# Optimization experiments

Measured on AMD Instinct MI355X. Metric: run time of the kernel, lower is better.

Reference implementation:

```python
import jax, jax.numpy as jnp
import numpy as np
from jax import lax

CONV3_NUM = 5
CONV1_NUM = 1
NEG_SLOPE = 0.2


def _leaky(x):
    return jnp.where(x >= 0, x, NEG_SLOPE * x)


def _per_sample_conv(x, k, b, pad):
    # x: [B,3,H,W], k: [B,3,3,kh,kw] (OIHW per sample), b: [B,3]
    def one(xi, ki, bi):
        y = lax.conv_general_dilated(
            xi[None], ki, (1, 1), ((pad, pad), (pad, pad)),
            dimension_numbers=("NCHW", "OIHW", "NCHW"))[0]
        return y + bi[:, None, None]
    return jax.vmap(one)(x, k, b)


def _conv3x3_block(x, feat):
    B = x.shape[0]
    k = feat[:, :81].reshape(B, 3, 3, 3, 3)
    b = feat[:, 81:84]
    return _leaky(x + _per_sample_conv(x, k, b, 1))


def _conv1x1_block(x, feat):
    B = x.shape[0]
    k = feat[:, :9].reshape(B, 3, 3, 1, 1)
    b = feat[:, 9:12]
    return _leaky(x + _per_sample_conv(x, k, b, 0))


def _att_map(f, h, w, xi):
    # f: [B,20]; h,w: [1,1,H,W]; xi: [B,1,H,W]  -> cubic trivariate polynomial
    c = lambda i: f[:, i][:, None, None, None]
    h2 = h * h; h3 = h2 * h
    w2 = w * w; w3 = w2 * w
    x2 = xi * xi; x3 = x2 * xi
    return (c(0) * h3 + c(1) * h2 * w + c(2) * h2 * xi + c(3) * h2
            + c(4) * h * w2 + c(5) * h * w * xi + c(6) * h * w
            + c(7) * h * x2 + c(8) * h * xi + c(9) * h
            + c(10) * w3 + c(11) * w2 * xi + c(12) * w2
            + c(13) * w * x2 + c(14) * w * xi + c(15) * w
            + c(16) * x3 + c(17) * x2 + c(18) * xi + c(19))


def setup_inputs() -> dict:
    key = jax.random.key(0)
    k1, k2, k3 = jax.random.split(key, 3)
    x = jax.random.normal(k1, (8, 3, 1024, 1024), dtype=jnp.float32)
    thumb_x = jax.random.normal(k2, (8, 3, 256, 256), dtype=jnp.float32)
    # meta() is an external CNN predicting per-sample params; we materialize its
    # output directly (scaled small for numerical stability of the conv stack).
    feature = jax.random.normal(k3, (8, 492), dtype=jnp.float32) * 0.05
    return {"x": x, "thumb_x": thumb_x, "feature": feature}


def reference(x, thumb_x, feature):
    B, _, H, W = x.shape
    residual = x
    for i in range(CONV3_NUM):
        x = _conv3x3_block(x, feature[:, i * 84:(i + 1) * 84])
    off = CONV3_NUM * 84
    for i in range(CONV1_NUM):
        x = _conv1x1_block(x, feature[:, off + i * 12:off + (i + 1) * 12])
    off = off + CONV1_NUM * 12
    x = residual + x
    dt = x.dtype
    h_mat = jnp.broadcast_to((jnp.arange(H, dtype=dt) / H)[None, None, :, None], (1, 1, H, W))
    w_mat = jnp.broadcast_to((jnp.arange(W, dtype=dt) / W)[None, None, None, :], (1, 1, H, W))
    atts = [_att_map(feature[:, off + 20 * c:off + 20 * (c + 1)], h_mat, w_mat, x[:, c:c + 1])
            for c in range(3)]
    att = jnp.concatenate(atts, axis=1)
    x = x * (1 + att)
    # location is None => thumbnail branch is skipped, thumb_x returned as-is
    return (x, thumb_x)
```

## Files before the change

kernel.cpp:

```cpp
#include <hip/hip_runtime.h>
#include <hip/hip_fp16.h>

typedef unsigned int uint;
typedef _Float16 h2 __attribute__((ext_vector_type(2)));


#define ROWS   42
#define W_U    40
#define W_REAL 38
#define CHP_U  (ROWS*W_U)
#define BUF_U  (3*CHP_U)

__device__ __forceinline__ h2   U2H(uint u) { return __builtin_bit_cast(h2, u); }
__device__ __forceinline__ uint H2U(h2 h)   { return __builtin_bit_cast(uint, h); }

__global__ void prep_weights(const float* __restrict__ feat, uint* __restrict__ wtab)
{
    const int b = blockIdx.x;
    const int t = threadIdx.x;
    float w = 0.f;
    bool valid = false;
    if (t < 405) {
        int l = t / 81, r = t % 81;
        int ic = r / 27; r %= 27;
        int ky = r / 9;  r %= 9;
        int oc = r / 3;
        int kx = r % 3;
        w = feat[b * 492 + l * 84 + ((oc * 3 + ic) * 3 + ky) * 3 + kx];
        valid = true;
    } else if (t < 420) {
        int i = t - 405;
        w = feat[b * 492 + (i / 3) * 84 + 81 + (i % 3)];
        valid = true;
    }
    if (valid) {
        _Float16 h = (_Float16)w;
        h2 hh = { h, h };
        wtab[b * 448 + t] = H2U(hh);
    }
}

__global__ __launch_bounds__(512, 8) void fused_net(
    const float* __restrict__ xin,
    const float* __restrict__ thumb,
    const float* __restrict__ feat,
    const uint*  __restrict__ wtab,
    float* __restrict__ out)
{
    const int tid = threadIdx.x;

    if (blockIdx.x == 16) {
        const int part = blockIdx.y + 32 * blockIdx.z;
        const float4* s4 = (const float4*)thumb;
        float4* d4 = (float4*)(out + 25165824ull);
        const int n4 = 1572864 / 4;
        for (int i = part * 512 + tid; i < n4; i += 256 * 512)
            d4[i] = s4[i];
        return;
    }

    const int gx0 = blockIdx.x * 64;
    const int gy0 = blockIdx.y * 32;
    const int b   = blockIdx.z;
    const bool edge = (gx0 == 0) | (gx0 == 960) | (gy0 == 0) | (gy0 == 992);
    const float* wf = feat + b * 492;
    const uint*  wt = wtab + b * 448;

    __shared__ __align__(16) uint lds[2 * BUF_U + 8];
    uint* b0 = lds;
    uint* b1 = lds + BUF_U + 4;

    const float* xb = xin + ((size_t)(b * 3) << 20);
    {
        int srow = tid / 38;
        int su   = tid - srow * 38;
        int sch  = 0;
        if (!edge) {
            #pragma unroll
            for (int it = 0; it < 10; ++it) {
                if (it < 9 || tid < 180) {
                    const float2 f = *(const float2*)(xb + ((size_t)sch << 20) +
                                                      ((size_t)(gy0 - 5 + srow) << 10) +
                                                      (gx0 - 6 + 2 * su));
                    b0[sch * CHP_U + srow * W_U + su] =
                        __builtin_bit_cast(uint, __builtin_amdgcn_cvt_pkrtz(f.x, f.y));
                }
                su += 18; srow += 13;
                if (su >= 38)   { su -= 38; srow += 1; }
                if (srow >= 42) { srow -= 42; sch += 1; }
            }
        } else {
            #pragma unroll
            for (int it = 0; it < 10; ++it) {
                if (it < 9 || tid < 180) {
                    const int gy = gy0 - 5 + srow;
                    const int gx = gx0 - 6 + 2 * su;
                    float2 f = {0.f, 0.f};
                    if ((unsigned)gy < 1024u && (unsigned)gx < 1024u)
                        f = *(const float2*)(xb + ((size_t)sch << 20) +
                                             ((size_t)gy << 10) + gx);
                    b0[sch * CHP_U + srow * W_U + su] =
                        __builtin_bit_cast(uint, __builtin_amdgcn_cvt_pkrtz(f.x, f.y));
                }
                su += 18; srow += 13;
                if (su >= 38)   { su -= 38; srow += 1; }
                if (srow >= 42) { srow -= 42; sch += 1; }
            }
        }
    }
    __syncthreads();

    const int er  = tid >> 5;
    const int uc  = tid & 31;
    const int ub0 = (5 + er) * W_U + 3 + uc;
    const int ub1 = ub0 + 16 * W_U;
    uint resu[2][3];
    #pragma unroll
    for (int ch = 0; ch < 3; ++ch) {
        resu[0][ch] = b0[ch * CHP_U + ub0];
        resu[1][ch] = b0[ch * CHP_U + ub1];
    }

    const int cr = tid / 18;
    const int cc = tid - cr * 18;
    const int y0 = 1 + 2 * cr;
    const int x0 = 2 + 4 * cc;
    uint mA[2] = {~0u, ~0u}, mB[2] = {~0u, ~0u};
    if (edge) {
        const int gyA = gy0 - 5 + y0;
        const int gxA = gx0 - 6 + x0;
        const uint mA0 = ((((unsigned)gxA       < 1024u) ? 0x0000ffffu : 0u) |
                          (((unsigned)(gxA + 1) < 1024u) ? 0xffff0000u : 0u));
        const uint mB0 = ((((unsigned)(gxA + 2) < 1024u) ? 0x0000ffffu : 0u) |
                          (((unsigned)(gxA + 3) < 1024u) ? 0xffff0000u : 0u));
        #pragma unroll
        for (int j = 0; j < 2; ++j) {
            const uint mr = ((unsigned)(gyA + j) < 1024u) ? ~0u : 0u;
            mA[j] = mA0 & mr;
            mB[j] = mB0 & mr;
        }
    }

    const h2 c02 = { (_Float16)0.2f, (_Float16)0.2f };

    #pragma unroll
    for (int l = 0; l < 5; ++l) {
        const uint* sb = (l & 1) ? b1 : b0;
        uint*       db = (l & 1) ? b0 : b1;
        if (tid < 360) {
            const uint* tb = sb + (y0 - 1) * W_U + 2 * cc;
            uint*       ob = db + y0 * W_U + 1 + 2 * cc;
            h2 accA[2][3], accB[2][3];
            #pragma unroll
            for (int oc = 0; oc < 3; ++oc) {
                const h2 bi = U2H(wt[405 + l * 3 + oc]);
                accA[0][oc] = bi; accA[1][oc] = bi;
                accB[0][oc] = bi; accB[1][oc] = bi;
            }
            #pragma unroll
            for (int ic = 0; ic < 3; ++ic) {
                #pragma unroll
                for (int t = 0; t < 4; ++t) {
                    const uint2 P = *(const uint2*)(tb + ic * CHP_U + t * W_U);
                    const uint2 Q = *(const uint2*)(tb + ic * CHP_U + t * W_U + 2);
                    const uint u0 = P.x, u1 = P.y, u2 = Q.x, u3 = Q.y;
                    const h2 X01 = U2H((u0 >> 16) | (u1 << 16));
                    const h2 C1  = U2H(u1);
                    const h2 X12 = U2H((u1 >> 16) | (u2 << 16));
                    const h2 C2  = U2H(u2);
                    const h2 X23 = U2H((u2 >> 16) | (u3 << 16));
                    #pragma unroll
                    for (int j = 0; j < 2; ++j) {
                        const int ky = t - j;
                        if (0 <= ky && ky <= 2) {
                            const int wb = l * 81 + (ic * 3 + ky) * 9;
                            #pragma unroll
                            for (int oc = 0; oc < 3; ++oc) {
                                const h2 w0 = U2H(wt[wb + oc * 3 + 0]);
                                const h2 w1 = U2H(wt[wb + oc * 3 + 1]);
                                const h2 w2 = U2H(wt[wb + oc * 3 + 2]);
                                accA[j][oc] = __builtin_elementwise_fma(w0, X01, accA[j][oc]);
                                accA[j][oc] = __builtin_elementwise_fma(w1, C1,  accA[j][oc]);
                                accA[j][oc] = __builtin_elementwise_fma(w2, X12, accA[j][oc]);
                                accB[j][oc] = __builtin_elementwise_fma(w0, X12, accB[j][oc]);
                                accB[j][oc] = __builtin_elementwise_fma(w1, C2,  accB[j][oc]);
                                accB[j][oc] = __builtin_elementwise_fma(w2, X23, accB[j][oc]);
                            }
                        }
                    }
                    if (t == 1) { accA[0][ic] = accA[0][ic] + C1; accB[0][ic] = accB[0][ic] + C2; }
                    if (t == 2) { accA[1][ic] = accA[1][ic] + C1; accB[1][ic] = accB[1][ic] + C2; }
                }
            }
            if (!edge) {
                #pragma unroll
                for (int j = 0; j < 2; ++j) {
                    #pragma unroll
                    for (int oc = 0; oc < 3; ++oc) {
                        h2 vA = accA[j][oc]; vA = __builtin_elementwise_max(vA, c02 * vA);
                        h2 vB = accB[j][oc]; vB = __builtin_elementwise_max(vB, c02 * vB);
                        ob[oc * CHP_U + j * W_U]     = H2U(vA);
                        ob[oc * CHP_U + j * W_U + 1] = H2U(vB);
                    }
                }
            } else {
                #pragma unroll
                for (int j = 0; j < 2; ++j) {
                    #pragma unroll
                    for (int oc = 0; oc < 3; ++oc) {
                        h2 vA = accA[j][oc]; vA = __builtin_elementwise_max(vA, c02 * vA);
                        h2 vB = accB[j][oc]; vB = __builtin_elementwise_max(vB, c02 * vB);
                        ob[oc * CHP_U + j * W_U]     = H2U(vA) & mA[j];
                        ob[oc * CHP_U + j * W_U + 1] = H2U(vB) & mB[j];
                    }
                }
            }
        }
        __syncthreads();
    }

    float* outb = out + ((size_t)(b * 3) << 20);
    #pragma unroll
    for (int rr = 0; rr < 2; ++rr) {
        const int ub = rr ? ub1 : ub0;
        const int gy = gy0 + er + 16 * rr;
        float x5f[3][2], resf[3][2];
        #pragma unroll
        for (int ch = 0; ch < 3; ++ch) {
            h2 hr = U2H(resu[rr][ch]);
            resf[ch][0] = (float)hr.x; resf[ch][1] = (float)hr.y;
            h2 hx = U2H(b1[ch * CHP_U + ub]);
            x5f[ch][0] = (float)hx.x; x5f[ch][1] = (float)hx.y;
        }
        const float h1 = (float)gy * (1.0f / 1024.0f);
        const float h2v = h1 * h1, h3 = h2v * h1;
        float tmp[3][2];
        #pragma unroll
        for (int j = 0; j < 2; ++j) {
            const float wc = (float)(gx0 + 2 * uc + j) * (1.0f / 1024.0f);
            const float w2 = wc * wc, w3 = w2 * wc;
            const float hw = h1 * wc, h2w = h2v * wc, hw2 = h1 * w2;
            #pragma unroll
            for (int oc = 0; oc < 3; ++oc) {
                float s = x5f[oc][j] + wf[429 + oc]
                        + wf[420 + oc * 3 + 0] * x5f[0][j]
                        + wf[420 + oc * 3 + 1] * x5f[1][j]
                        + wf[420 + oc * 3 + 2] * x5f[2][j];
                s = s >= 0.f ? s : 0.2f * s;
                const float xf = resf[oc][j] + s;
                const float x1 = xf, x2 = x1 * x1, x3 = x2 * x1;
                const float* cf = wf + 432 + oc * 20;
                float att =
                    cf[0] * h3 + cf[1] * h2w + cf[2] * h2v * x1 + cf[3] * h2v +
                    cf[4] * hw2 + cf[5] * hw * x1 + cf[6] * hw + cf[7] * h1 * x2 +
                    cf[8] * h1 * x1 + cf[9] * h1 + cf[10] * w3 + cf[11] * w2 * x1 +
                    cf[12] * w2 + cf[13] * wc * x2 + cf[14] * wc * x1 + cf[15] * wc +
                    cf[16] * x3 + cf[17] * x2 + cf[18] * x1 + cf[19];
                tmp[oc][j] = xf * (1.f + att);
            }
        }
        #pragma unroll
        for (int oc = 0; oc < 3; ++oc) {
            float2 v = {tmp[oc][0], tmp[oc][1]};
            *(float2*)&outb[((size_t)oc << 20) + ((size_t)gy << 10) + (gx0 + 2 * uc)] = v;
        }
    }
}

extern "C" void kernel_launch(void* const* d_in, const int* in_sizes, int n_in,
                              void* d_out, int out_size, void* d_ws, size_t ws_size,
                              hipStream_t stream) {
    const float* x     = (const float*)d_in[0];
    const float* thumb = (const float*)d_in[1];
    const float* feat  = (const float*)d_in[2];
    float* out = (float*)d_out;
    uint* wtab = (uint*)d_ws;

    prep_weights<<<dim3(8), 448, 0, stream>>>(feat, wtab);
    dim3 grid(17, 32, 8);
    fused_net<<<grid, 512, 0, stream>>>(x, thumb, feat, wtab, out);
}
```

Before: 288.4 us.

## Widen tiles to 128 columns and fuse final conv layer with epilogue

Doubles the tile width from 64 to 128 columns using 1024-thread blocks. The halo recomputation overhead per output pixel drops from roughly 42x76 to 42x140 loaded per 32x128 output. The fifth conv layer now applies the 1x1 block, residual and attention polynomial directly from registers and writes global memory. This removes the last LDS write, a barrier and the separate epilogue pass. The cost is larger LDS per block and fewer resident blocks, plus uneven work among threads in the final layer.

```diff
diff --git a/kernel.cpp b/kernel.cpp
--- a/kernel.cpp
+++ b/kernel.cpp
@@ -6,10 +6,11 @@
 
 
 #define ROWS   42
-#define W_U    40
-#define W_REAL 38
+#define W_U    72
+#define W_REAL 70
 #define CHP_U  (ROWS*W_U)
 #define BUF_U  (3*CHP_U)
+#define NST    680
 
 __device__ __forceinline__ h2   U2H(uint u) { return __builtin_bit_cast(h2, u); }
 __device__ __forceinline__ uint H2U(h2 h)   { return __builtin_bit_cast(uint, h); }
@@ -40,7 +41,7 @@
     }
 }
 
-__global__ __launch_bounds__(512, 8) void fused_net(
+__global__ __launch_bounds__(1024, 8) void fused_net(
     const float* __restrict__ xin,
     const float* __restrict__ thumb,
     const float* __restrict__ feat,
@@ -49,20 +50,20 @@
 {
     const int tid = threadIdx.x;
 
-    if (blockIdx.x == 16) {
+    if (blockIdx.x == 8) {
         const int part = blockIdx.y + 32 * blockIdx.z;
         const float4* s4 = (const float4*)thumb;
         float4* d4 = (float4*)(out + 25165824ull);
         const int n4 = 1572864 / 4;
-        for (int i = part * 512 + tid; i < n4; i += 256 * 512)
+        for (int i = part * 1024 + tid; i < n4; i += 256 * 1024)
             d4[i] = s4[i];
         return;
     }
 
-    const int gx0 = blockIdx.x * 64;
+    const int gx0 = blockIdx.x * 128;
     const int gy0 = blockIdx.y * 32;
     const int b   = blockIdx.z;
-    const bool edge = (gx0 == 0) | (gx0 == 960) | (gy0 == 0) | (gy0 == 992);
+    const bool edge = (gx0 == 0) | (gx0 == 896) | (gy0 == 0) | (gy0 == 992);
     const float* wf = feat + b * 492;
     const uint*  wt = wtab + b * 448;
 
@@ -72,27 +73,27 @@
 
     const float* xb = xin + ((size_t)(b * 3) << 20);
     {
-        int srow = tid / 38;
-        int su   = tid - srow * 38;
+        int srow = tid / 70;
+        int su   = tid - srow * 70;
         int sch  = 0;
         if (!edge) {
             #pragma unroll
-            for (int it = 0; it < 10; ++it) {
-                if (it < 9 || tid < 180) {
+            for (int it = 0; it < 9; ++it) {
+                if (it < 8 || tid < 628) {
                     const float2 f = *(const float2*)(xb + ((size_t)sch << 20) +
                                                       ((size_t)(gy0 - 5 + srow) << 10) +
                                                       (gx0 - 6 + 2 * su));
                     b0[sch * CHP_U + srow * W_U + su] =
                         __builtin_bit_cast(uint, __builtin_amdgcn_cvt_pkrtz(f.x, f.y));
                 }
-                su += 18; srow += 13;
-                if (su >= 38)   { su -= 38; srow += 1; }
+                su += 44; srow += 14;
+                if (su >= 70)   { su -= 70; srow += 1; }
                 if (srow >= 42) { srow -= 42; sch += 1; }
             }
         } else {
             #pragma unroll
-            for (int it = 0; it < 10; ++it) {
-                if (it < 9 || tid < 180) {
+            for (int it = 0; it < 9; ++it) {
+                if (it < 8 || tid < 628) {
                     const int gy = gy0 - 5 + srow;
                     const int gx = gx0 - 6 + 2 * su;
                     float2 f = {0.f, 0.f};
@@ -102,29 +103,31 @@
                     b0[sch * CHP_U + srow * W_U + su] =
                         __builtin_bit_cast(uint, __builtin_amdgcn_cvt_pkrtz(f.x, f.y));
                 }
-                su += 18; srow += 13;
-                if (su >= 38)   { su -= 38; srow += 1; }
+                su += 44; srow += 14;
+                if (su >= 70)   { su -= 70; srow += 1; }
                 if (srow >= 42) { srow -= 42; sch += 1; }
             }
         }
     }
     __syncthreads();
 
-    const int er  = tid >> 5;
-    const int uc  = tid & 31;
-    const int ub0 = (5 + er) * W_U + 3 + uc;
-    const int ub1 = ub0 + 16 * W_U;
-    uint resu[2][3];
-    #pragma unroll
-    for (int ch = 0; ch < 3; ++ch) {
-        resu[0][ch] = b0[ch * CHP_U + ub0];
-        resu[1][ch] = b0[ch * CHP_U + ub1];
-    }
-
-    const int cr = tid / 18;
-    const int cc = tid - cr * 18;
+    const int cr = tid / 34;
+    const int cc = tid - cr * 34;
     const int y0 = 1 + 2 * cr;
     const int x0 = 2 + 4 * cc;
+    const bool ep = (tid < NST) & (cr >= 2) & (cr <= 17) & (cc >= 1) & (cc <= 32);
+
+    uint resA[3][2], resB[3][2];
+    if (ep) {
+        #pragma unroll
+        for (int ch = 0; ch < 3; ++ch)
+            #pragma unroll
+            for (int j = 0; j < 2; ++j) {
+                resA[ch][j] = b0[ch * CHP_U + (y0 + j) * W_U + 1 + 2 * cc];
+                resB[ch][j] = b0[ch * CHP_U + (y0 + j) * W_U + 2 + 2 * cc];
+            }
+    }
+
     uint mA[2] = {~0u, ~0u}, mB[2] = {~0u, ~0u};
     if (edge) {
         const int gyA = gy0 - 5 + y0;
@@ -147,9 +150,9 @@
     for (int l = 0; l < 5; ++l) {
         const uint* sb = (l & 1) ? b1 : b0;
         uint*       db = (l & 1) ? b0 : b1;
-        if (tid < 360) {
+        const bool act = (l < 4) ? (tid < NST) : ep;
+        if (act) {
             const uint* tb = sb + (y0 - 1) * W_U + 2 * cc;
-            uint*       ob = db + y0 * W_U + 1 + 2 * cc;
             h2 accA[2][3], accB[2][3];
             #pragma unroll
             for (int oc = 0; oc < 3; ++oc) {
@@ -192,78 +195,87 @@
                     if (t == 2) { accA[1][ic] = accA[1][ic] + C1; accB[1][ic] = accB[1][ic] + C2; }
                 }
             }
-            if (!edge) {
+            #pragma unroll
+            for (int j = 0; j < 2; ++j)
+                #pragma unroll
+                for (int oc = 0; oc < 3; ++oc) {
+                    accA[j][oc] = __builtin_elementwise_max(accA[j][oc], c02 * accA[j][oc]);
+                    accB[j][oc] = __builtin_elementwise_max(accB[j][oc], c02 * accB[j][oc]);
+                }
+
+            if (l < 4) {
+                uint* ob = db + y0 * W_U + 1 + 2 * cc;
+                if (!edge) {
+                    #pragma unroll
+                    for (int j = 0; j < 2; ++j)
+                        #pragma unroll
+                        for (int oc = 0; oc < 3; ++oc) {
+                            ob[oc * CHP_U + j * W_U]     = H2U(accA[j][oc]);
+                            ob[oc * CHP_U + j * W_U + 1] = H2U(accB[j][oc]);
+                        }
+                } else {
+                    #pragma unroll
+                    for (int j = 0; j < 2; ++j)
+                        #pragma unroll
+                        for (int oc = 0; oc < 3; ++oc) {
+                            ob[oc * CHP_U + j * W_U]     = H2U(accA[j][oc]) & mA[j];
+                            ob[oc * CHP_U + j * W_U + 1] = H2U(accB[j][oc]) & mB[j];
+                        }
+                }
+            } else {
+                const int gxA = gx0 - 6 + x0;
+                float* outb = out + ((size_t)(b * 3) << 20);
                 #pragma unroll
                 for (int j = 0; j < 2; ++j) {
-                    #pragma unroll
-                    for (int oc = 0; oc < 3; ++oc) {
-                        h2 vA = accA[j][oc]; vA = __builtin_elementwise_max(vA, c02 * vA);
-                        h2 vB = accB[j][oc]; vB = __builtin_elementwise_max(vB, c02 * vB);
-                        ob[oc * CHP_U + j * W_U]     = H2U(vA);
-                        ob[oc * CHP_U + j * W_U + 1] = H2U(vB);
+                    const int gy = gy0 - 5 + y0 + j;
+                    const float h1 = (float)gy * (1.0f / 1024.0f);
+                    const float h2v = h1 * h1, h3 = h2v * h1;
+                    #pragma unroll
+                    for (int hh = 0; hh < 2; ++hh) {
+                        float x5[3][2], rs[3][2];
+                        #pragma unroll
+                        for (int ch = 0; ch < 3; ++ch) {
+                            const h2 a = hh ? accB[j][ch] : accA[j][ch];
+                            x5[ch][0] = (float)a.x; x5[ch][1] = (float)a.y;
+                            const h2 r = U2H(hh ? resB[ch][j] : resA[ch][j]);
+                            rs[ch][0] = (float)r.x; rs[ch][1] = (float)r.y;
+                        }
+                        float o[3][2];
+                        #pragma unroll
+                        for (int p = 0; p < 2; ++p) {
+                            const float wc = (float)(gxA + 2 * hh + p) * (1.0f / 1024.0f);
+                            const float w2 = wc * wc, w3 = w2 * wc;
+                            const float hw = h1 * wc, h2w = h2v * wc, hw2 = h1 * w2;
+                            #pragma unroll
+                            for (int oc = 0; oc < 3; ++oc) {
+                                float s = x5[oc][p] + wf[429 + oc]
+                                        + wf[420 + oc * 3 + 0] * x5[0][p]
+                                        + wf[420 + oc * 3 + 1] * x5[1][p]
+                                        + wf[420 + oc * 3 + 2] * x5[2][p];
+                                s = s >= 0.f ? s : 0.2f * s;
+                                const float xf = rs[oc][p] + s;
+                                const float x1 = xf, x2 = x1 * x1, x3 = x2 * x1;
+                                const float* cf = wf + 432 + oc * 20;
+                                float att =
+                                    cf[0] * h3 + cf[1] * h2w + cf[2] * h2v * x1 + cf[3] * h2v +
+                                    cf[4] * hw2 + cf[5] * hw * x1 + cf[6] * hw + cf[7] * h1 * x2 +
+                                    cf[8] * h1 * x1 + cf[9] * h1 + cf[10] * w3 + cf[11] * w2 * x1 +
+                                    cf[12] * w2 + cf[13] * wc * x2 + cf[14] * wc * x1 + cf[15] * wc +
+                                    cf[16] * x3 + cf[17] * x2 + cf[18] * x1 + cf[19];
+                                o[oc][p] = xf * (1.f + att);
+                            }
+                        }
+                        #pragma unroll
+                        for (int oc = 0; oc < 3; ++oc) {
+                            float2 v = {o[oc][0], o[oc][1]};
+                            *(float2*)&outb[((size_t)oc << 20) + ((size_t)gy << 10) +
+                                            (gxA + 2 * hh)] = v;
+                        }
                     }
                 }
-            } else {
-                #pragma unroll
-                for (int j = 0; j < 2; ++j) {
-                    #pragma unroll
-                    for (int oc = 0; oc < 3; ++oc) {
-                        h2 vA = accA[j][oc]; vA = __builtin_elementwise_max(vA, c02 * vA);
-                        h2 vB = accB[j][oc]; vB = __builtin_elementwise_max(vB, c02 * vB);
-                        ob[oc * CHP_U + j * W_U]     = H2U(vA) & mA[j];
-                        ob[oc * CHP_U + j * W_U + 1] = H2U(vB) & mB[j];
-                    }
-                }
             }
         }
-        __syncthreads();
-    }
-
-    float* outb = out + ((size_t)(b * 3) << 20);
-    #pragma unroll
-    for (int rr = 0; rr < 2; ++rr) {
-        const int ub = rr ? ub1 : ub0;
-        const int gy = gy0 + er + 16 * rr;
-        float x5f[3][2], resf[3][2];
-        #pragma unroll
-        for (int ch = 0; ch < 3; ++ch) {
-            h2 hr = U2H(resu[rr][ch]);
-            resf[ch][0] = (float)hr.x; resf[ch][1] = (float)hr.y;
-            h2 hx = U2H(b1[ch * CHP_U + ub]);
-            x5f[ch][0] = (float)hx.x; x5f[ch][1] = (float)hx.y;
-        }
-        const float h1 = (float)gy * (1.0f / 1024.0f);
-        const float h2v = h1 * h1, h3 = h2v * h1;
-        float tmp[3][2];
-        #pragma unroll
-        for (int j = 0; j < 2; ++j) {
-            const float wc = (float)(gx0 + 2 * uc + j) * (1.0f / 1024.0f);
-            const float w2 = wc * wc, w3 = w2 * wc;
-            const float hw = h1 * wc, h2w = h2v * wc, hw2 = h1 * w2;
-            #pragma unroll
-            for (int oc = 0; oc < 3; ++oc) {
-                float s = x5f[oc][j] + wf[429 + oc]
-                        + wf[420 + oc * 3 + 0] * x5f[0][j]
-                        + wf[420 + oc * 3 + 1] * x5f[1][j]
-                        + wf[420 + oc * 3 + 2] * x5f[2][j];
-                s = s >= 0.f ? s : 0.2f * s;
-                const float xf = resf[oc][j] + s;
-                const float x1 = xf, x2 = x1 * x1, x3 = x2 * x1;
-                const float* cf = wf + 432 + oc * 20;
-                float att =
-                    cf[0] * h3 + cf[1] * h2w + cf[2] * h2v * x1 + cf[3] * h2v +
-                    cf[4] * hw2 + cf[5] * hw * x1 + cf[6] * hw + cf[7] * h1 * x2 +
-                    cf[8] * h1 * x1 + cf[9] * h1 + cf[10] * w3 + cf[11] * w2 * x1 +
-                    cf[12] * w2 + cf[13] * wc * x2 + cf[14] * wc * x1 + cf[15] * wc +
-                    cf[16] * x3 + cf[17] * x2 + cf[18] * x1 + cf[19];
-                tmp[oc][j] = xf * (1.f + att);
-            }
-        }
-        #pragma unroll
-        for (int oc = 0; oc < 3; ++oc) {
-            float2 v = {tmp[oc][0], tmp[oc][1]};
-            *(float2*)&outb[((size_t)oc << 20) + ((size_t)gy << 10) + (gx0 + 2 * uc)] = v;
-        }
+        if (l < 4) __syncthreads();
     }
 }
 
@@ -277,6 +289,6 @@
     uint* wtab = (uint*)d_ws;
 
     prep_weights<<<dim3(8), 448, 0, stream>>>(feat, wtab);
-    dim3 grid(17, 32, 8);
-    fused_net<<<grid, 512, 0, stream>>>(x, thumb, feat, wtab, out);
+    dim3 grid(9, 32, 8);
+    fused_net<<<grid, 1024, 0, stream>>>(x, thumb, feat, wtab, out);
 }
```

Result: slower. 307.9 us (+6.8%).

## Process two vertical tiles per block with register-prefetched second halo

Applied to the files above, without the earlier changes.

Each block now covers a 64-row strip as two 32-row halves, halving the grid in y. The second half's input halo is loaded from global memory into registers before the first half's conv stack runs, then converted and written to shared memory afterwards, so the load latency overlaps with compute. This costs extra registers (20 floats per thread) and halves the number of blocks, which may reduce occupancy or load balance. The thumbnail copy blocks are rescaled to match the new grid.

```diff
diff --git a/kernel.cpp b/kernel.cpp
--- a/kernel.cpp
+++ b/kernel.cpp
@@ -13,6 +13,10 @@
 
 __device__ __forceinline__ h2   U2H(uint u) { return __builtin_bit_cast(h2, u); }
 __device__ __forceinline__ uint H2U(h2 h)   { return __builtin_bit_cast(uint, h); }
+
+#define ADV_WALK() do { su += 18; srow += 13;                  \
+                        if (su >= 38)   { su -= 38; srow += 1; } \
+                        if (srow >= 42) { srow -= 42; sch += 1; } } while (0)
 
 __global__ void prep_weights(const float* __restrict__ feat, uint* __restrict__ wtab)
 {
@@ -50,19 +54,21 @@
     const int tid = threadIdx.x;
 
     if (blockIdx.x == 16) {
-        const int part = blockIdx.y + 32 * blockIdx.z;
+        const int part = blockIdx.y + 16 * blockIdx.z;
         const float4* s4 = (const float4*)thumb;
         float4* d4 = (float4*)(out + 25165824ull);
         const int n4 = 1572864 / 4;
-        for (int i = part * 512 + tid; i < n4; i += 256 * 512)
+        for (int i = part * 512 + tid; i < n4; i += 128 * 512)
             d4[i] = s4[i];
         return;
     }
 
     const int gx0 = blockIdx.x * 64;
-    const int gy0 = blockIdx.y * 32;
+    const int gy0 = blockIdx.y * 64;
     const int b   = blockIdx.z;
-    const bool edge = (gx0 == 0) | (gx0 == 960) | (gy0 == 0) | (gy0 == 992);
+    const bool xedge = (gx0 == 0) | (gx0 == 960);
+    const bool edge0 = xedge | (blockIdx.y == 0);
+    const bool edge1 = xedge | (blockIdx.y == 15);
     const float* wf = feat + b * 492;
     const uint*  wt = wtab + b * 448;
 
@@ -71,11 +77,12 @@
     uint* b1 = lds + BUF_U + 4;
 
     const float* xb = xin + ((size_t)(b * 3) << 20);
+
     {
         int srow = tid / 38;
         int su   = tid - srow * 38;
         int sch  = 0;
-        if (!edge) {
+        if (!edge0) {
             #pragma unroll
             for (int it = 0; it < 10; ++it) {
                 if (it < 9 || tid < 180) {
@@ -85,9 +92,7 @@
                     b0[sch * CHP_U + srow * W_U + su] =
                         __builtin_bit_cast(uint, __builtin_amdgcn_cvt_pkrtz(f.x, f.y));
                 }
-                su += 18; srow += 13;
-                if (su >= 38)   { su -= 38; srow += 1; }
-                if (srow >= 42) { srow -= 42; sch += 1; }
+                ADV_WALK();
             }
         } else {
             #pragma unroll
@@ -102,167 +107,216 @@
                     b0[sch * CHP_U + srow * W_U + su] =
                         __builtin_bit_cast(uint, __builtin_amdgcn_cvt_pkrtz(f.x, f.y));
                 }
-                su += 18; srow += 13;
-                if (su >= 38)   { su -= 38; srow += 1; }
-                if (srow >= 42) { srow -= 42; sch += 1; }
+                ADV_WALK();
             }
         }
     }
     __syncthreads();
+
+    float2 pre[10];
+    {
+        int srow = tid / 38;
+        int su   = tid - srow * 38;
+        int sch  = 0;
+        const int gyb = gy0 + 27;
+        if (!edge1) {
+            #pragma unroll
+            for (int it = 0; it < 10; ++it) {
+                if (it < 9 || tid < 180)
+                    pre[it] = *(const float2*)(xb + ((size_t)sch << 20) +
+                                               ((size_t)(gyb + srow) << 10) +
+                                               (gx0 - 6 + 2 * su));
+                ADV_WALK();
+            }
+        } else {
+            #pragma unroll
+            for (int it = 0; it < 10; ++it) {
+                pre[it].x = 0.f; pre[it].y = 0.f;
+                if (it < 9 || tid < 180) {
+                    const int gy = gyb + srow;
+                    const int gx = gx0 - 6 + 2 * su;
+                    if ((unsigned)gy < 1024u && (unsigned)gx < 1024u)
+                        pre[it] = *(const float2*)(xb + ((size_t)sch << 20) +
+                                                   ((size_t)gy << 10) + gx);
+                }
+                ADV_WALK();
+            }
+        }
+    }
 
     const int er  = tid >> 5;
     const int uc  = tid & 31;
     const int ub0 = (5 + er) * W_U + 3 + uc;
     const int ub1 = ub0 + 16 * W_U;
-    uint resu[2][3];
-    #pragma unroll
-    for (int ch = 0; ch < 3; ++ch) {
-        resu[0][ch] = b0[ch * CHP_U + ub0];
-        resu[1][ch] = b0[ch * CHP_U + ub1];
-    }
-
     const int cr = tid / 18;
     const int cc = tid - cr * 18;
     const int y0 = 1 + 2 * cr;
     const int x0 = 2 + 4 * cc;
-    uint mA[2] = {~0u, ~0u}, mB[2] = {~0u, ~0u};
-    if (edge) {
-        const int gyA = gy0 - 5 + y0;
-        const int gxA = gx0 - 6 + x0;
-        const uint mA0 = ((((unsigned)gxA       < 1024u) ? 0x0000ffffu : 0u) |
-                          (((unsigned)(gxA + 1) < 1024u) ? 0xffff0000u : 0u));
-        const uint mB0 = ((((unsigned)(gxA + 2) < 1024u) ? 0x0000ffffu : 0u) |
-                          (((unsigned)(gxA + 3) < 1024u) ? 0xffff0000u : 0u));
+
+    const h2 c02 = { (_Float16)0.2f, (_Float16)0.2f };
+    float* outb = out + ((size_t)(b * 3) << 20);
+
+    #pragma unroll 1
+    for (int half = 0; half < 2; ++half) {
+        const int  gy0h  = gy0 + 32 * half;
+        const bool edgeh = half ? edge1 : edge0;
+
+        uint resu[2][3];
         #pragma unroll
-        for (int j = 0; j < 2; ++j) {
-            const uint mr = ((unsigned)(gyA + j) < 1024u) ? ~0u : 0u;
-            mA[j] = mA0 & mr;
-            mB[j] = mB0 & mr;
-        }
-    }
-
-    const h2 c02 = { (_Float16)0.2f, (_Float16)0.2f };
-
-    #pragma unroll
-    for (int l = 0; l < 5; ++l) {
-        const uint* sb = (l & 1) ? b1 : b0;
-        uint*       db = (l & 1) ? b0 : b1;
-        if (tid < 360) {
-            const uint* tb = sb + (y0 - 1) * W_U + 2 * cc;
-            uint*       ob = db + y0 * W_U + 1 + 2 * cc;
-            h2 accA[2][3], accB[2][3];
-            #pragma unroll
-            for (int oc = 0; oc < 3; ++oc) {
-                const h2 bi = U2H(wt[405 + l * 3 + oc]);
-                accA[0][oc] = bi; accA[1][oc] = bi;
-                accB[0][oc] = bi; accB[1][oc] = bi;
-            }
-            #pragma unroll
-            for (int ic = 0; ic < 3; ++ic) {
+        for (int ch = 0; ch < 3; ++ch) {
+            resu[0][ch] = b0[ch * CHP_U + ub0];
+            resu[1][ch] = b0[ch * CHP_U + ub1];
+        }
+
+        uint mA[2] = {~0u, ~0u}, mB[2] = {~0u, ~0u};
+        if (edgeh) {
+            const int gyA = gy0h - 5 + y0;
+            const int gxA = gx0 - 6 + x0;
+            const uint mA0 = ((((unsigned)gxA       < 1024u) ? 0x0000ffffu : 0u) |
+                              (((unsigned)(gxA + 1) < 1024u) ? 0xffff0000u : 0u));
+            const uint mB0 = ((((unsigned)(gxA + 2) < 1024u) ? 0x0000ffffu : 0u) |
+                              (((unsigned)(gxA + 3) < 1024u) ? 0xffff0000u : 0u));
+            #pragma unroll
+            for (int j = 0; j < 2; ++j) {
+                const uint mr = ((unsigned)(gyA + j) < 1024u) ? ~0u : 0u;
+                mA[j] = mA0 & mr;
+                mB[j] = mB0 & mr;
+            }
+        }
+
+        #pragma unroll
+        for (int l = 0; l < 5; ++l) {
+            const uint* sb = (l & 1) ? b1 : b0;
+            uint*       db = (l & 1) ? b0 : b1;
+            if (tid < 360) {
+                const uint* tb = sb + (y0 - 1) * W_U + 2 * cc;
+                uint*       ob = db + y0 * W_U + 1 + 2 * cc;
+                h2 accA[2][3], accB[2][3];
                 #pragma unroll
-                for (int t = 0; t < 4; ++t) {
-                    const uint2 P = *(const uint2*)(tb + ic * CHP_U + t * W_U);
-                    const uint2 Q = *(const uint2*)(tb + ic * CHP_U + t * W_U + 2);
-                    const uint u0 = P.x, u1 = P.y, u2 = Q.x, u3 = Q.y;
-                    const h2 X01 = U2H((u0 >> 16) | (u1 << 16));
-                    const h2 C1  = U2H(u1);
-                    const h2 X12 = U2H((u1 >> 16) | (u2 << 16));
-                    const h2 C2  = U2H(u2);
-                    const h2 X23 = U2H((u2 >> 16) | (u3 << 16));
+                for (int oc = 0; oc < 3; ++oc) {
+                    const h2 bi = U2H(wt[405 + l * 3 + oc]);
+                    accA[0][oc] = bi; accA[1][oc] = bi;
+                    accB[0][oc] = bi; accB[1][oc] = bi;
+                }
+                #pragma unroll
+                for (int ic = 0; ic < 3; ++ic) {
                     #pragma unroll
-                    for (int j = 0; j < 2; ++j) {
-                        const int ky = t - j;
-                        if (0 <= ky && ky <= 2) {
-                            const int wb = l * 81 + (ic * 3 + ky) * 9;
-                            #pragma unroll
-                            for (int oc = 0; oc < 3; ++oc) {
-                                const h2 w0 = U2H(wt[wb + oc * 3 + 0]);
-                                const h2 w1 = U2H(wt[wb + oc * 3 + 1]);
-                                const h2 w2 = U2H(wt[wb + oc * 3 + 2]);
-                                accA[j][oc] = __builtin_elementwise_fma(w0, X01, accA[j][oc]);
-                                accA[j][oc] = __builtin_elementwise_fma(w1, C1,  accA[j][oc]);
-                                accA[j][oc] = __builtin_elementwise_fma(w2, X12, accA[j][oc]);
-                                accB[j][oc] = __builtin_elementwise_fma(w0, X12, accB[j][oc]);
-                                accB[j][oc] = __builtin_elementwise_fma(w1, C2,  accB[j][oc]);
-                                accB[j][oc] = __builtin_elementwise_fma(w2, X23, accB[j][oc]);
+                    for (int t = 0; t < 4; ++t) {
+                        const uint2 P = *(const uint2*)(tb + ic * CHP_U + t * W_U);
+                        const uint2 Q = *(const uint2*)(tb + ic * CHP_U + t * W_U + 2);
+                        const uint u0 = P.x, u1 = P.y, u2 = Q.x, u3 = Q.y;
+                        const h2 X01 = U2H((u0 >> 16) | (u1 << 16));
+                        const h2 C1  = U2H(u1);
+                        const h2 X12 = U2H((u1 >> 16) | (u2 << 16));
+                        const h2 C2  = U2H(u2);
+                        const h2 X23 = U2H((u2 >> 16) | (u3 << 16));
+                        #pragma unroll
+                        for (int j = 0; j < 2; ++j) {
+                            const int ky = t - j;
+                            if (0 <= ky && ky <= 2) {
+                                const int wb = l * 81 + (ic * 3 + ky) * 9;
+                                #pragma unroll
+                                for (int oc = 0; oc < 3; ++oc) {
+                                    const h2 w0 = U2H(wt[wb + oc * 3 + 0]);
+                                    const h2 w1 = U2H(wt[wb + oc * 3 + 1]);
+                                    const h2 w2 = U2H(wt[wb + oc * 3 + 2]);
+                                    accA[j][oc] = __builtin_elementwise_fma(w0, X01, accA[j][oc]);
+                                    accA[j][oc] = __builtin_elementwise_fma(w1, C1,  accA[j][oc]);
+                                    accA[j][oc] = __builtin_elementwise_fma(w2, X12, accA[j][oc]);
+                                    accB[j][oc] = __builtin_elementwise_fma(w0, X12, accB[j][oc]);
+                                    accB[j][oc] = __builtin_elementwise_fma(w1, C2,  accB[j][oc]);
+                                    accB[j][oc] = __builtin_elementwise_fma(w2, X23, accB[j][oc]);
+                                }
                             }
                         }
+                        if (t == 1) { accA[0][ic] = accA[0][ic] + C1; accB[0][ic] = accB[0][ic] + C2; }
+                        if (t == 2) { accA[1][ic] = accA[1][ic] + C1; accB[1][ic] = accB[1][ic] + C2; }
                     }
-                    if (t == 1) { accA[0][ic] = accA[0][ic] + C1; accB[0][ic] = accB[0][ic] + C2; }
-                    if (t == 2) { accA[1][ic] = accA[1][ic] + C1; accB[1][ic] = accB[1][ic] + C2; }
-                }
-            }
-            if (!edge) {
+                }
+                if (!edgeh) {
+                    #pragma unroll
+                    for (int j = 0; j < 2; ++j)
+                        #pragma unroll
+                        for (int oc = 0; oc < 3; ++oc) {
+                            h2 vA = accA[j][oc]; vA = __builtin_elementwise_max(vA, c02 * vA);
+                            h2 vB = accB[j][oc]; vB = __builtin_elementwise_max(vB, c02 * vB);
+                            ob[oc * CHP_U + j * W_U]     = H2U(vA);
+                            ob[oc * CHP_U + j * W_U + 1] = H2U(vB);
+                        }
+                } else {
+                    #pragma unroll
+                    for (int j = 0; j < 2; ++j)
+                        #pragma unroll
+                        for (int oc = 0; oc < 3; ++oc) {
+                            h2 vA = accA[j][oc]; vA = __builtin_elementwise_max(vA, c02 * vA);
+                            h2 vB = accB[j][oc]; vB = __builtin_elementwise_max(vB, c02 * vB);
+                            ob[oc * CHP_U + j * W_U]     = H2U(vA) & mA[j];
+                            ob[oc * CHP_U + j * W_U + 1] = H2U(vB) & mB[j];
+                        }
+                }
+            }
+            __syncthreads();
+        }
+
+        #pragma unroll
+        for (int rr = 0; rr < 2; ++rr) {
+            const int ub = rr ? ub1 : ub0;
+            const int gy = gy0h + er + 16 * rr;
+            float x5f[3][2], resf[3][2];
+            #pragma unroll
+            for (int ch = 0; ch < 3; ++ch) {
+                h2 hr = U2H(resu[rr][ch]);
+                resf[ch][0] = (float)hr.x; resf[ch][1] = (float)hr.y;
+                h2 hx = U2H(b1[ch * CHP_U + ub]);
+                x5f[ch][0] = (float)hx.x; x5f[ch][1] = (float)hx.y;
+            }
+            const float h1 = (float)gy * (1.0f / 1024.0f);
+            const float h2v = h1 * h1, h3 = h2v * h1;
+            float tmp[3][2];
+            #pragma unroll
+            for (int j = 0; j < 2; ++j) {
+                const float wc = (float)(gx0 + 2 * uc + j) * (1.0f / 1024.0f);
+                const float w2 = wc * wc, w3 = w2 * wc;
+                const float hw = h1 * wc, h2w = h2v * wc, hw2 = h1 * w2;
                 #pragma unroll
-                for (int j = 0; j < 2; ++j) {
-                    #pragma unroll
-                    for (int oc = 0; oc < 3; ++oc) {
-                        h2 vA = accA[j][oc]; vA = __builtin_elementwise_max(vA, c02 * vA);
-                        h2 vB = accB[j][oc]; vB = __builtin_elementwise_max(vB, c02 * vB);
-                        ob[oc * CHP_U + j * W_U]     = H2U(vA);
-                        ob[oc * CHP_U + j * W_U + 1] = H2U(vB);
-                    }
-                }
-            } else {
-                #pragma unroll
-                for (int j = 0; j < 2; ++j) {
-                    #pragma unroll
-                    for (int oc = 0; oc < 3; ++oc) {
-                        h2 vA = accA[j][oc]; vA = __builtin_elementwise_max(vA, c02 * vA);
-                        h2 vB = accB[j][oc]; vB = __builtin_elementwise_max(vB, c02 * vB);
-                        ob[oc * CHP_U + j * W_U]     = H2U(vA) & mA[j];
-                        ob[oc * CHP_U + j * W_U + 1] = H2U(vB) & mB[j];
-                    }
-                }
-            }
-        }
-        __syncthreads();
-    }
-
-    float* outb = out + ((size_t)(b * 3) << 20);
-    #pragma unroll
-    for (int rr = 0; rr < 2; ++rr) {
-        const int ub = rr ? ub1 : ub0;
-        const int gy = gy0 + er + 16 * rr;
-        float x5f[3][2], resf[3][2];
-        #pragma unroll
-        for (int ch = 0; ch < 3; ++ch) {
-            h2 hr = U2H(resu[rr][ch]);
-            resf[ch][0] = (float)hr.x; resf[ch][1] = (float)hr.y;
-            h2 hx = U2H(b1[ch * CHP_U + ub]);
-            x5f[ch][0] = (float)hx.x; x5f[ch][1] = (float)hx.y;
-        }
-        const float h1 = (float)gy * (1.0f / 1024.0f);
-        const float h2v = h1 * h1, h3 = h2v * h1;
-        float tmp[3][2];
-        #pragma unroll
-        for (int j = 0; j < 2; ++j) {
-            const float wc = (float)(gx0 + 2 * uc + j) * (1.0f / 1024.0f);
-            const float w2 = wc * wc, w3 = w2 * wc;
-            const float hw = h1 * wc, h2w = h2v * wc, hw2 = h1 * w2;
+                for (int oc = 0; oc < 3; ++oc) {
+                    float s = x5f[oc][j] + wf[429 + oc]
+                            + wf[420 + oc * 3 + 0] * x5f[0][j]
+                            + wf[420 + oc * 3 + 1] * x5f[1][j]
+                            + wf[420 + oc * 3 + 2] * x5f[2][j];
+                    s = s >= 0.f ? s : 0.2f * s;
+                    const float xf = resf[oc][j] + s;
+                    const float x1 = xf, x2 = x1 * x1, x3 = x2 * x1;
+                    const float* cf = wf + 432 + oc * 20;
+                    float att =
+                        cf[0] * h3 + cf[1] * h2w + cf[2] * h2v * x1 + cf[3] * h2v +
+                        cf[4] * hw2 + cf[5] * hw * x1 + cf[6] * hw + cf[7] * h1 * x2 +
+                        cf[8] * h1 * x1 + cf[9] * h1 + cf[10] * w3 + cf[11] * w2 * x1 +
+                        cf[12] * w2 + cf[13] * wc * x2 + cf[14] * wc * x1 + cf[15] * wc +
+                        cf[16] * x3 + cf[17] * x2 + cf[18] * x1 + cf[19];
+                    tmp[oc][j] = xf * (1.f + att);
+                }
+            }
             #pragma unroll
             for (int oc = 0; oc < 3; ++oc) {
-                float s = x5f[oc][j] + wf[429 + oc]
-                        + wf[420 + oc * 3 + 0] * x5f[0][j]
-                        + wf[420 + oc * 3 + 1] * x5f[1][j]
-                        + wf[420 + oc * 3 + 2] * x5f[2][j];
-                s = s >= 0.f ? s : 0.2f * s;
-                const float xf = resf[oc][j] + s;
-                const float x1 = xf, x2 = x1 * x1, x3 = x2 * x1;
-                const float* cf = wf + 432 + oc * 20;
-                float att =
-                    cf[0] * h3 + cf[1] * h2w + cf[2] * h2v * x1 + cf[3] * h2v +
-                    cf[4] * hw2 + cf[5] * hw * x1 + cf[6] * hw + cf[7] * h1 * x2 +
-                    cf[8] * h1 * x1 + cf[9] * h1 + cf[10] * w3 + cf[11] * w2 * x1 +
-                    cf[12] * w2 + cf[13] * wc * x2 + cf[14] * wc * x1 + cf[15] * wc +
-                    cf[16] * x3 + cf[17] * x2 + cf[18] * x1 + cf[19];
-                tmp[oc][j] = xf * (1.f + att);
-            }
-        }
-        #pragma unroll
-        for (int oc = 0; oc < 3; ++oc) {
-            float2 v = {tmp[oc][0], tmp[oc][1]};
-            *(float2*)&outb[((size_t)oc << 20) + ((size_t)gy << 10) + (gx0 + 2 * uc)] = v;
+                float2 v = {tmp[oc][0], tmp[oc][1]};
+                *(float2*)&outb[((size_t)oc << 20) + ((size_t)gy << 10) + (gx0 + 2 * uc)] = v;
+            }
+        }
+
+        if (half == 0) {
+            __syncthreads();
+            int srow = tid / 38;
+            int su   = tid - srow * 38;
+            int sch  = 0;
+            #pragma unroll
+            for (int it = 0; it < 10; ++it) {
+                if (it < 9 || tid < 180)
+                    b0[sch * CHP_U + srow * W_U + su] =
+                        __builtin_bit_cast(uint, __builtin_amdgcn_cvt_pkrtz(pre[it].x, pre[it].y));
+                ADV_WALK();
+            }
+            __syncthreads();
         }
     }
 }
@@ -277,6 +331,6 @@
     uint* wtab = (uint*)d_ws;
 
     prep_weights<<<dim3(8), 448, 0, stream>>>(feat, wtab);
-    dim3 grid(17, 32, 8);
+    dim3 grid(17, 16, 8);
     fused_net<<<grid, 512, 0, stream>>>(x, thumb, feat, wtab, out);
 }
```

Result: slower. 382.7 us (+32.7%).
